# Kernel tuning notes

Measured on AMD Instinct MI355X. Metric: run time of the kernel, lower is better.

## Reference

```python
import jax, jax.numpy as jnp
import numpy as np

# SLAYER SRMALPHA neuron / simulation parameters (network.yaml)
THETA = 10.0      # spike threshold
TAU_SR = 10.0     # synaptic (psp) time constant
TAU_REF = 1.0     # refractory time constant
SCALE_REF = 2.0   # refractory scale (kernel mult = -scaleRef*theta)
TS = 1.0          # simulation step
K_SR = 100        # truncation length of srm (psp) kernel
K_REF = 32        # truncation length of refractory kernel
B, C_IN, C_OUT, T = 512, 39 * 2 * 2, 50, 325


def _alpha_kernel(tau, mult, length):
    t = jnp.arange(length, dtype=jnp.float32)
    return mult * (t / tau) * jnp.exp(1.0 - t / tau)  # k[0] == 0


def _psp(x, kernel):
    """Causal temporal filter: y[t] = sum_s kernel[s] * x[t-s]. x: [B,C,T]."""
    b, c, t = x.shape
    k = kernel.shape[0]
    w = kernel[::-1].reshape(1, 1, k)
    y = jax.lax.conv_general_dilated(
        x.reshape(b * c, 1, t), w, (1,), [(k - 1, 0)],
        dimension_numbers=('NCH', 'OIH', 'NCH'))
    return y.reshape(b, c, t)


@jax.custom_vjp
def _spike(v):
    return (v >= THETA).astype(v.dtype)

def _spike_fwd(v):
    return _spike(v), v

def _spike_bwd(v, g):
    # SLAYER surrogate gradient rho(v) = (scaleRho/theta) * exp(-tauRho*|v-theta|/theta)
    rho = (1.0 / THETA) * jnp.exp(-jnp.abs(v - THETA) / THETA)
    return (g * rho,)

_spike.defvjp(_spike_fwd, _spike_bwd)


def setup_inputs() -> dict:
    key = jax.random.key(0)
    k1, k2 = jax.random.split(key)
    spike_input = jax.random.uniform(k1, (B, C_IN, T), dtype=jnp.float32)
    weight = jax.random.normal(k2, (C_OUT, C_IN), dtype=jnp.float32) / np.sqrt(C_IN)
    return {"spike_input": spike_input, "weight": weight}


def reference(spike_input, weight):
    eps = _alpha_kernel(TAU_SR, 1.0, K_SR)                 # synaptic kernel
    nu = _alpha_kernel(TAU_REF, -SCALE_REF * THETA, K_REF)  # refractory kernel

    psp = _psp(spike_input, eps)                 # [B, 156, T]
    u_in = jnp.einsum('bct,oc->bot', psp, weight)  # [B, 50, T], bias-free dense

    u_seq = jnp.moveaxis(u_in, -1, 0)            # [T, B, 50]
    b, o = u_seq.shape[1], u_seq.shape[2]
    ref0 = jnp.zeros((b, o, K_REF), u_in.dtype)  # future refractory contributions
    nu_tail = nu[1:]                             # nu[0] == 0

    def step(ref, u):
        v = u + ref[..., 0]                      # membrane potential at t
        s = _spike(v)                            # LIF threshold
        ref = jnp.concatenate(
            [ref[..., 1:] + s[..., None] * nu_tail,
             jnp.zeros((b, o, 1), u.dtype)], axis=-1)
        return ref, s

    _, spikes = jax.lax.scan(step, ref0, u_seq)  # [T, B, 50]
    return jnp.moveaxis(spikes, 0, -1) / TS      # [B, 50, T]
```

## Files before the change

kernel.cpp:

```cpp
#include <hip/hip_runtime.h>
#include <math.h>

#define B_    512
#define CIN_  156
#define COUT_ 50
#define T_    325
#define KSR_  100
#define XSZ   (B_*CIN_*T_)

#define PASSES 4
#define NBP    (B_/PASSES)

#define EPS_OFF 0
#define NU_OFF  512
#define PSP_OFF 4096
#define U_OFF   (4096 + NBP*CIN_*T_*4)

__global__ __launch_bounds__(128) void k_setup(char* __restrict__ ws) {
  float* eps = (float*)(ws + EPS_OFF);
  float* nu  = (float*)(ws + NU_OFF);
  int tid = threadIdx.x;
  if (tid < KSR_) {
    float q   = (float)((double)tid / 10.0);
    float arg = __fsub_rn(1.0f, q);
    float E   = (float)exp((double)arg);
    eps[tid]  = __fmul_rn(q, E);
  }
  if (tid >= 64 && tid < 96) {
    int s = tid - 64;
    float m   = -20.0f * (float)s;
    float E   = (float)exp((double)(1 - s));
    nu[s]     = __fmul_rn(m, E);
  }
}

__global__ __launch_bounds__(256) void k_conv(const float* __restrict__ x,
                                              const float* __restrict__ eps,
                                              float* __restrict__ psp,
                                              int b0) {
  __shared__ float ly[4][436];
  int wv = threadIdx.x >> 6, lane = threadIdx.x & 63;
  int row = blockIdx.x * 4 + wv;
  const float* xr = x + (size_t)(b0 * CIN_ + row) * T_;
  float* l = ly[wv];
  for (int i = lane; i < 436; i += 64) l[i] = 0.0f;
  for (int i = lane; i < T_; i += 64) l[99 + i] = xr[i];
  __syncthreads();
  int tb = lane * 6;
  if (tb < T_) {
    float acc[6] = {0, 0, 0, 0, 0, 0};
    float win[6];
#pragma unroll
    for (int j = 0; j < 6; ++j) win[j] = l[99 + tb + j];
#pragma unroll
    for (int s = 0; s < KSR_; ++s) {
      float e = eps[s];
#pragma unroll
      for (int j = 0; j < 6; ++j)
        acc[j] = __fadd_rn(acc[j], __fmul_rn(e, win[j]));
      if (s < KSR_ - 1) {
#pragma unroll
        for (int j = 5; j >= 1; --j) win[j] = win[j - 1];
        win[0] = l[98 + tb - s];
      }
    }
    float* pr = psp + (size_t)row * T_;
#pragma unroll
    for (int j = 0; j < 6; ++j)
      if (tb + j < T_) pr[tb + j] = acc[j];
  }
}

__global__ __launch_bounds__(256) void k_matmul(const float* __restrict__ psp,
                                                const float* __restrict__ w,
                                                float* __restrict__ u) {
  unsigned tid = blockIdx.x * 256u + threadIdx.x;
  if (tid >= (unsigned)(NBP * T_)) return;
  unsigned bl = tid / (unsigned)T_;
  unsigned t  = tid - bl * (unsigned)T_;
  const float* pp = psp + (size_t)bl * (CIN_ * T_) + t;
  float acc[COUT_];
#pragma unroll
  for (int o = 0; o < COUT_; ++o) acc[o] = 0.0f;
  for (int c = 0; c < CIN_; ++c) {
    float pv = pp[(size_t)c * T_];
#pragma unroll
    for (int o = 0; o < COUT_; ++o)
      acc[o] = __fadd_rn(acc[o], __fmul_rn(w[o * CIN_ + c], pv));
  }
  float* up = u + (size_t)bl * (COUT_ * T_) + t;
#pragma unroll
  for (int o = 0; o < COUT_; ++o) up[(size_t)o * T_] = acc[o];
}

__global__ __launch_bounds__(64) void k_scan(const float* __restrict__ u,
                                             const float* __restrict__ nu,
                                             float* __restrict__ out,
                                             int row0) {
  int bl = blockIdx.x * 64 + threadIdx.x;
  const float* up = u + (size_t)bl * T_;
  float* op = out + (size_t)(row0 + bl) * T_;
  float nt[31], r[31];
#pragma unroll
  for (int k = 0; k < 31; ++k) { nt[k] = nu[k + 1]; r[k] = 0.0f; }
#pragma unroll 5
  for (int t = 0; t < T_; ++t) {
    float v = __fadd_rn(up[t], r[0]);
    bool s = (v >= 10.0f);
    float sf = s ? 1.0f : 0.0f;
#pragma unroll
    for (int k = 0; k < 30; ++k)
      r[k] = __fadd_rn(r[k + 1], __fmul_rn(sf, nt[k]));
    r[30] = __fmul_rn(sf, nt[30]);
    op[t] = sf;
  }
}

extern "C" void kernel_launch(void* const* d_in, const int* in_sizes, int n_in,
                              void* d_out, int out_size, void* d_ws, size_t ws_size,
                              hipStream_t stream) {
  int xi = (in_sizes[0] == XSZ) ? 0 : 1;
  const float* x = (const float*)d_in[xi];
  const float* w = (const float*)d_in[1 - xi];
  char* ws = (char*)d_ws;
  float* out = (float*)d_out;

  const float* eps = (const float*)(ws + EPS_OFF);
  const float* nu  = (const float*)(ws + NU_OFF);
  float* psp       = (float*)(ws + PSP_OFF);
  float* u         = (float*)(ws + U_OFF);

  k_setup<<<1, 128, 0, stream>>>(ws);
  for (int p = 0; p < PASSES; ++p) {
    int b0 = p * NBP;
    int conv_blocks = (NBP * CIN_) / 4;
    int mm_blocks   = (NBP * T_ + 255) / 256;
    int scan_blocks = (NBP * COUT_) / 64;
    k_conv<<<conv_blocks, 256, 0, stream>>>(x, eps, psp, b0);
    k_matmul<<<mm_blocks, 256, 0, stream>>>(psp, w, u);
    k_scan<<<scan_blocks, 64, 0, stream>>>(u, nu, out, b0 * COUT_);
  }
}
```

Before: 763.2 us.

## Split matmul outputs across threads, batch scan once, prefetch conv window from LDS

The matmul kernel now gives each thread 5 of the 50 output channels, so it launches ten times more threads with far fewer live accumulators. This targets the low occupancy and register pressure of the 50-accumulator version. The u buffer now holds the full batch so the scan runs once at the end with 400 blocks instead of four small launches. The conv kernel software-prefetches its LDS window in chunks of ten and adds a barrier between zeroing and filling. The trade-off is that each psp value is re-read ten times from global or cache, and the u workspace grows to the full batch size.

```diff
diff --git a/kernel.cpp b/kernel.cpp
--- a/kernel.cpp
+++ b/kernel.cpp
@@ -10,11 +10,13 @@
 
 #define PASSES 4
 #define NBP    (B_/PASSES)
+#define OSPLIT 10
+#define OG     (COUT_/OSPLIT)
 
 #define EPS_OFF 0
 #define NU_OFF  512
 #define PSP_OFF 4096
-#define U_OFF   (4096 + NBP*CIN_*T_*4)
+#define U_OFF   (PSP_OFF + NBP*CIN_*T_*4)
 
 __global__ __launch_bounds__(128) void k_setup(char* __restrict__ ws) {
   float* eps = (float*)(ws + EPS_OFF);
@@ -38,31 +40,46 @@
                                               const float* __restrict__ eps,
                                               float* __restrict__ psp,
                                               int b0) {
-  __shared__ float ly[4][436];
+  __shared__ float ly[4][440];
   int wv = threadIdx.x >> 6, lane = threadIdx.x & 63;
   int row = blockIdx.x * 4 + wv;
   const float* xr = x + (size_t)(b0 * CIN_ + row) * T_;
   float* l = ly[wv];
-  for (int i = lane; i < 436; i += 64) l[i] = 0.0f;
-  for (int i = lane; i < T_; i += 64) l[99 + i] = xr[i];
+  for (int i = lane; i < 440; i += 64) l[i] = 0.0f;
+  __syncthreads();
+  for (int i = lane; i < T_; i += 64) l[103 + i] = xr[i];
   __syncthreads();
   int tb = lane * 6;
   if (tb < T_) {
     float acc[6] = {0, 0, 0, 0, 0, 0};
     float win[6];
 #pragma unroll
-    for (int j = 0; j < 6; ++j) win[j] = l[99 + tb + j];
+    for (int j = 0; j < 6; ++j) win[j] = l[103 + tb + j];
+    float ecur[10], enx[10];
 #pragma unroll
-    for (int s = 0; s < KSR_; ++s) {
-      float e = eps[s];
+    for (int k = 0; k < 10; ++k) ecur[k] = l[103 + tb - k];
 #pragma unroll
-      for (int j = 0; j < 6; ++j)
-        acc[j] = __fadd_rn(acc[j], __fmul_rn(e, win[j]));
-      if (s < KSR_ - 1) {
+    for (int chunk = 0; chunk < 10; ++chunk) {
+      if (chunk < 9) {
 #pragma unroll
-        for (int j = 5; j >= 1; --j) win[j] = win[j - 1];
-        win[0] = l[98 + tb - s];
+        for (int k = 0; k < 10; ++k)
+          enx[k] = l[103 + tb - (chunk + 1) * 10 - k];
       }
+#pragma unroll
+      for (int k = 0; k < 10; ++k) {
+        int s = chunk * 10 + k;
+        if (s > 0) {
+#pragma unroll
+          for (int j = 5; j >= 1; --j) win[j] = win[j - 1];
+          win[0] = ecur[k];
+        }
+        float e = eps[s];
+#pragma unroll
+        for (int j = 0; j < 6; ++j)
+          acc[j] = __fadd_rn(acc[j], __fmul_rn(e, win[j]));
+      }
+#pragma unroll
+      for (int k = 0; k < 10; ++k) ecur[k] = enx[k];
     }
     float* pr = psp + (size_t)row * T_;
 #pragma unroll
@@ -73,33 +90,36 @@
 
 __global__ __launch_bounds__(256) void k_matmul(const float* __restrict__ psp,
                                                 const float* __restrict__ w,
-                                                float* __restrict__ u) {
+                                                float* __restrict__ u,
+                                                int b0) {
   unsigned tid = blockIdx.x * 256u + threadIdx.x;
-  if (tid >= (unsigned)(NBP * T_)) return;
-  unsigned bl = tid / (unsigned)T_;
-  unsigned t  = tid - bl * (unsigned)T_;
+  unsigned og  = tid / (unsigned)(NBP * T_);
+  unsigned rem = tid - og * (unsigned)(NBP * T_);
+  unsigned bl  = rem / (unsigned)T_;
+  unsigned t   = rem - bl * (unsigned)T_;
   const float* pp = psp + (size_t)bl * (CIN_ * T_) + t;
-  float acc[COUT_];
+  const float* wr = w + og * OG * CIN_;
+  float acc[OG];
 #pragma unroll
-  for (int o = 0; o < COUT_; ++o) acc[o] = 0.0f;
+  for (int j = 0; j < OG; ++j) acc[j] = 0.0f;
+#pragma unroll 4
   for (int c = 0; c < CIN_; ++c) {
     float pv = pp[(size_t)c * T_];
 #pragma unroll
-    for (int o = 0; o < COUT_; ++o)
-      acc[o] = __fadd_rn(acc[o], __fmul_rn(w[o * CIN_ + c], pv));
+    for (int j = 0; j < OG; ++j)
+      acc[j] = __fadd_rn(acc[j], __fmul_rn(wr[j * CIN_ + c], pv));
   }
-  float* up = u + (size_t)bl * (COUT_ * T_) + t;
+  float* up = u + ((size_t)(b0 + bl) * COUT_ + og * OG) * T_ + t;
 #pragma unroll
-  for (int o = 0; o < COUT_; ++o) up[(size_t)o * T_] = acc[o];
+  for (int j = 0; j < OG; ++j) up[(size_t)j * T_] = acc[j];
 }
 
 __global__ __launch_bounds__(64) void k_scan(const float* __restrict__ u,
                                              const float* __restrict__ nu,
-                                             float* __restrict__ out,
-                                             int row0) {
-  int bl = blockIdx.x * 64 + threadIdx.x;
-  const float* up = u + (size_t)bl * T_;
-  float* op = out + (size_t)(row0 + bl) * T_;
+                                             float* __restrict__ out) {
+  int row = blockIdx.x * 64 + threadIdx.x;
+  const float* up = u + (size_t)row * T_;
+  float* op = out + (size_t)row * T_;
   float nt[31], r[31];
 #pragma unroll
   for (int k = 0; k < 31; ++k) { nt[k] = nu[k + 1]; r[k] = 0.0f; }
@@ -133,11 +153,8 @@
   k_setup<<<1, 128, 0, stream>>>(ws);
   for (int p = 0; p < PASSES; ++p) {
     int b0 = p * NBP;
-    int conv_blocks = (NBP * CIN_) / 4;
-    int mm_blocks   = (NBP * T_ + 255) / 256;
-    int scan_blocks = (NBP * COUT_) / 64;
-    k_conv<<<conv_blocks, 256, 0, stream>>>(x, eps, psp, b0);
-    k_matmul<<<mm_blocks, 256, 0, stream>>>(psp, w, u);
-    k_scan<<<scan_blocks, 64, 0, stream>>>(u, nu, out, b0 * COUT_);
+    k_conv<<<(NBP * CIN_) / 4, 256, 0, stream>>>(x, eps, psp, b0);
+    k_matmul<<<(OSPLIT * NBP * T_) / 256, 256, 0, stream>>>(psp, w, u, b0);
   }
+  k_scan<<<400, 64, 0, stream>>>(u, nu, out);
 }
```

Result: faster. 619.0 us (-18.9%).
